# Optimization experiments

Measured on AMD Instinct MI355X. Metric: run time of the kernel, lower is better.

The kernel has to match this reference:

```python
import jax, jax.numpy as jnp
import numpy as np

N, C, H, L = 10000, 256, 8, 3
D = C // H  # per-head dim
E = 320000


def setup_inputs() -> dict:
    key = jax.random.key(0)
    ks = jax.random.split(key, 12)
    x = jax.random.normal(ks[0], (N, C), dtype=jnp.float32)
    edge_index = jax.random.randint(ks[1], (2, E), 0, N, dtype=jnp.int64)
    s = 0.02
    Wq = jax.random.normal(ks[2], (L, C, C), dtype=jnp.float32) * s
    Wk = jax.random.normal(ks[3], (L, C, C), dtype=jnp.float32) * s
    Wv = jax.random.normal(ks[4], (L, C, C), dtype=jnp.float32) * s
    Ws = jax.random.normal(ks[5], (L, C, C), dtype=jnp.float32) * s
    bq = jax.random.normal(ks[6], (L, C), dtype=jnp.float32) * s
    bk = jax.random.normal(ks[7], (L, C), dtype=jnp.float32) * s
    bv = jax.random.normal(ks[8], (L, C), dtype=jnp.float32) * s
    bs = jax.random.normal(ks[9], (L, C), dtype=jnp.float32) * s
    return {"x": x, "Wq": Wq, "bq": bq, "Wk": Wk, "bk": bk,
            "Wv": Wv, "bv": bv, "Ws": Ws, "bs": bs, "edge_index": edge_index}


def _transformer_conv(x, Wq, bq, Wk, bk, Wv, bv, Ws, bs, src, dst):
    # projections: [N, C] -> [N, H, D]
    q = (x @ Wq + bq).reshape(N, H, D)
    k = (x @ Wk + bk).reshape(N, H, D)
    v = (x @ Wv + bv).reshape(N, H, D)
    # per-edge attention scores: query at target, key/value at source
    score = jnp.einsum('ehd,ehd->eh', q[dst], k[src]) / jnp.sqrt(jnp.float32(D))  # [E, H]
    # scatter softmax over incoming edges per target node
    m = jax.ops.segment_max(score, dst, num_segments=N)            # [N, H]
    a = jnp.exp(score - m[dst])                                    # [E, H]
    denom = jax.ops.segment_sum(a, dst, num_segments=N)           # [N, H]
    alpha = a / (denom[dst] + 1e-16)                               # [E, H]
    # weighted aggregation of values
    msg = alpha[:, :, None] * v[src]                               # [E, H, D]
    out = jax.ops.segment_sum(msg, dst, num_segments=N).reshape(N, C)
    # root/skip connection
    return out + x @ Ws + bs


def reference(x, Wq, bq, Wk, bk, Wv, bv, Ws, bs, edge_index):
    src, dst = edge_index[0], edge_index[1]
    for l in range(L):
        x = _transformer_conv(x, Wq[l], bq[l], Wk[l], bk[l],
                              Wv[l], bv[l], Ws[l], bs[l], src, dst)
    return x
```

## Files before the change

### kernel.cpp

```cpp
#include <hip/hip_runtime.h>
#include <hip/hip_bf16.h>

#define N_NODES 10000
#define C_DIM   256
#define H_HEADS 8
#define D_HEAD  32
#define E_EDGES 320000
#define L_LAYERS 3
#define GN      1024

typedef __attribute__((ext_vector_type(8))) short bf16x8;
typedef __attribute__((ext_vector_type(4))) float f32x4;

__device__ __forceinline__ unsigned short f2b(float f) {
  __hip_bfloat16 h = __float2bfloat16(f);
  return *(unsigned short*)&h;
}

__device__ __forceinline__ float kv_lo(unsigned int w) {
  union { unsigned int u; float f; } c; c.u = w << 16; return c.f;
}
__device__ __forceinline__ float kv_hi(unsigned int w) {
  union { unsigned int u; float f; } c; c.u = w & 0xffff0000u; return c.f;
}

__device__ __forceinline__ float red8(float p) {
  p += __shfl_xor(p, 1);
  p += __shfl_xor(p, 2);
  p += __shfl_xor(p, 4);
  return p;
}

__device__ __forceinline__ float dot4(float4 q, uint4 w) {
  return fmaf(q.x, kv_lo(w.x),
         fmaf(q.y, kv_lo(w.y),
         fmaf(q.z, kv_lo(w.z), q.w * kv_lo(w.w))));
}

__device__ __forceinline__ void gload16(const void* g, void* l) {
  __builtin_amdgcn_global_load_lds(
      (const __attribute__((address_space(1))) unsigned int*)g,
      (__attribute__((address_space(3))) unsigned int*)l, 16, 0, 0);
}

__device__ __forceinline__ int colmap(int mat, int c) {
  if (mat == 0) return c;
  if (mat == 3) return 768 + c;
  return 256 + ((c >> 6) << 7) + ((mat - 1) << 6) + (c & 63);
}

__global__ void hist_kernel(const int* __restrict__ dst, int* __restrict__ deg) {
  int e = blockIdx.x * blockDim.x + threadIdx.x;
  if (e < E_EDGES) atomicAdd(&deg[dst[e]], 1);
}

__global__ __launch_bounds__(1024) void scan_kernel(const int* __restrict__ deg,
                                                    int* __restrict__ row_ptr) {
  __shared__ int part[1024];
  int t = threadIdx.x;
  const int CHUNK = (N_NODES + 1023) / 1024;
  int base = t * CHUNK;
  int s = 0;
  for (int i = 0; i < CHUNK; ++i) {
    int idx = base + i;
    if (idx < N_NODES) s += deg[idx];
  }
  part[t] = s;
  __syncthreads();
  for (int off = 1; off < 1024; off <<= 1) {
    int v = (t >= off) ? part[t - off] : 0;
    __syncthreads();
    part[t] += v;
    __syncthreads();
  }
  int run = (t == 0) ? 0 : part[t - 1];
  for (int i = 0; i < CHUNK; ++i) {
    int idx = base + i;
    if (idx <= N_NODES) {
      row_ptr[idx] = run;
      if (idx < N_NODES) run += deg[idx];
    }
  }
}

__global__ void scatter_kernel(const int* __restrict__ src, const int* __restrict__ dst,
                               const int* __restrict__ row_ptr, int* __restrict__ fill,
                               int* __restrict__ srcs) {
  int e = blockIdx.x * blockDim.x + threadIdx.x;
  if (e < E_EDGES) {
    int d = dst[e];
    int pos = atomicAdd(&fill[d], 1);
    srcs[row_ptr[d] + pos] = src[e];
  }
}

__global__ __launch_bounds__(256) void conv_all_kernel(
    const float* __restrict__ x, __hip_bfloat16* __restrict__ xb,
    const float* __restrict__ Wq, const float* __restrict__ Wk,
    const float* __restrict__ Wv, const float* __restrict__ Ws,
    __hip_bfloat16* __restrict__ Wt,
    const float* __restrict__ bq, const float* __restrict__ bk,
    const float* __restrict__ bv, const float* __restrict__ bs,
    float* __restrict__ biasf) {
  __shared__ float tt[32][33];
  int b = blockIdx.x, t = threadIdx.x;
  if (b < 2500) {
    int i = b * 256 + t;
    float4 f = *(const float4*)&x[(size_t)i * 4];
    union { unsigned short u[4]; uint2 w; } o;
    o.u[0] = f2b(f.x); o.u[1] = f2b(f.y); o.u[2] = f2b(f.z); o.u[3] = f2b(f.w);
    *(uint2*)&xb[(size_t)i * 4] = o.w;
  } else if (b < 3268) {
    int zz = b - 2500;
    int z = zz >> 6, tile = zz & 63;
    int l = z >> 2, mat = z & 3;
    const float* W = (mat == 0 ? Wq : mat == 1 ? Wk : mat == 2 ? Wv : Ws)
                     + (size_t)l * C_DIM * C_DIM;
    int k0 = (tile >> 3) * 32, c0 = (tile & 7) * 32;
    int tx = t & 31, ty = t >> 5;
    for (int i = 0; i < 32; i += 8)
      tt[ty + i][tx] = W[(k0 + ty + i) * C_DIM + c0 + tx];
    __syncthreads();
    for (int i = 0; i < 32; i += 8) {
      int ncol = colmap(mat, c0 + ty + i);
      Wt[(size_t)l * GN * C_DIM + (size_t)ncol * C_DIM + k0 + tx] =
          __float2bfloat16(tt[tx][ty + i]);
    }
  } else {
    int i = (b - 3268) * 256 + t;
    if (i < L_LAYERS * GN) {
      int l = i >> 10, n = i & 1023;
      int mat = n >> 8, c = n & 255;
      const float* bb = (mat == 0 ? bq : mat == 1 ? bk : mat == 2 ? bv : bs);
      biasf[l * GN + colmap(mat, c)] = bb[l * C_DIM + c];
    }
  }
}

__global__ __launch_bounds__(256) void gemm_kernel(
    const __hip_bfloat16* __restrict__ xb,
    const __hip_bfloat16* __restrict__ Wt,
    const float* __restrict__ biasf,
    float* __restrict__ q4,
    unsigned short* __restrict__ kvu,
    float* __restrict__ skip) {
  __shared__ __align__(16) unsigned short SH[16384];
  __hip_bfloat16* As = (__hip_bfloat16*)SH;
  __hip_bfloat16* Bs = (__hip_bfloat16*)(SH + 8192);
  int tid = threadIdx.x;
  int wid = tid >> 6, lane = tid & 63;
  int row0 = blockIdx.x * 128;
  int col0 = blockIdx.y * 128;
  int wr = wid >> 1, wc = wid & 1;
  int lr = lane & 15, lq = lane >> 4;
  int swz = (lr & 7) * 8;

  f32x4 acc[4][4] = {};

  for (int k0 = 0; k0 < C_DIM; k0 += 64) {
#pragma unroll
    for (int j = 0; j < 4; ++j) {
      int c = j * 256 + wid * 64 + lane;
      int arow = c >> 3;
      int kc = 8 * ((c & 7) ^ ((c >> 3) & 7));
      int grow = row0 + arow;
      if (grow > N_NODES - 1) grow = N_NODES - 1;
      gload16(xb + (size_t)grow * C_DIM + k0 + kc, As + (size_t)(j * 256 + wid * 64) * 8);
    }
#pragma unroll
    for (int j = 0; j < 4; ++j) {
      int c = j * 256 + wid * 64 + lane;
      int brow = c >> 3;
      int kc = 8 * ((c & 7) ^ ((c >> 3) & 7));
      gload16(Wt + (size_t)(col0 + brow) * C_DIM + k0 + kc,
              Bs + (size_t)(j * 256 + wid * 64) * 8);
    }
    __syncthreads();

#pragma unroll
    for (int ks = 0; ks < 2; ++ks) {
      bf16x8 fa[4], fb[4];
#pragma unroll
      for (int m = 0; m < 4; ++m)
        fa[m] = *(const bf16x8*)&As[(wr * 64 + m * 16 + lr) * 64 + ((ks * 32 + lq * 8) ^ swz)];
#pragma unroll
      for (int n = 0; n < 4; ++n)
        fb[n] = *(const bf16x8*)&Bs[(wc * 64 + n * 16 + lr) * 64 + ((ks * 32 + lq * 8) ^ swz)];
#pragma unroll
      for (int m = 0; m < 4; ++m)
#pragma unroll
        for (int n = 0; n < 4; ++n)
          acc[m][n] = __builtin_amdgcn_mfma_f32_16x16x32_bf16(fa[m], fb[n], acc[m][n], 0, 0, 0);
    }
    __syncthreads();
  }

  float bias_n[4];
#pragma unroll
  for (int n = 0; n < 4; ++n) bias_n[n] = biasf[col0 + wc * 64 + n * 16 + lr];

  if (col0 >= 256 && col0 < 768) {
    int half = wc;
#pragma unroll
    for (int m = 0; m < 4; ++m) {
#pragma unroll
      for (int n = 0; n < 4; ++n) {
        int chs = n * 16 + lr;
#pragma unroll
        for (int r = 0; r < 4; ++r) {
          int row = wr * 64 + m * 16 + lq * 4 + r;
          SH[row * 128 + chs * 2 + half] = f2b(acc[m][n][r] + bias_n[n]);
        }
      }
    }
    __syncthreads();
    int slice = (col0 - 256) >> 7;
    unsigned int* kvd = (unsigned int*)kvu;
    int t16 = tid & 15, rbase = tid >> 4;
#pragma unroll
    for (int it = 0; it < 8; ++it) {
      int row = it * 16 + rbase;
      int grow = row0 + row;
      if (grow < N_NODES) {
        uint4 vv = *(const uint4*)&SH[row * 128 + t16 * 8];
        *(uint4*)&kvd[((size_t)slice * N_NODES + grow) * 64 + t16 * 4] = vv;
      }
    }
  } else {
#pragma unroll
    for (int m = 0; m < 4; ++m) {
#pragma unroll
      for (int n = 0; n < 4; ++n) {
        int colG = col0 + wc * 64 + n * 16 + lr;
#pragma unroll
        for (int r = 0; r < 4; ++r) {
          int grow = row0 + wr * 64 + m * 16 + lq * 4 + r;
          if (grow < N_NODES) {
            float val = acc[m][n][r] + bias_n[n];
            if (col0 < 256) {
              q4[((size_t)(colG >> 6) * N_NODES + grow) * 64 + (colG & 63)] = val;
            } else {
              skip[(size_t)grow * C_DIM + (colG - 768)] = val;
            }
          }
        }
      }
    }
  }
}

__global__ __launch_bounds__(256) void agg_kernel(
    const float* __restrict__ q4,
    const unsigned int* __restrict__ kv4,
    const int* __restrict__ row_ptr, const int* __restrict__ srcs,
    float* __restrict__ out, __hip_bfloat16* __restrict__ xb_next) {
  int b = blockIdx.x;
  int u = b >> 3, r = b & 7;
  int slice = r >> 1;
  int wid = threadIdx.x >> 6, lane = threadIdx.x & 63;
  int n = ((((u << 1) | (r & 1)) << 2) + wid);
  int slot = lane >> 4;
  int l4 = (lane & 15) * 4;
  const size_t SB = (size_t)slice * N_NODES * 64;
  const float scl = 0.25503526f;

  float4 qv = *(const float4*)&q4[SB + (size_t)n * 64 + l4];
  qv.x *= scl; qv.y *= scl; qv.z *= scl; qv.w *= scl;
  const unsigned int* kvs = kv4 + SB;

  int beg = row_ptr[n], end = row_ptr[n + 1];
  float l = 0.f;
  float4 a = make_float4(0.f, 0.f, 0.f, 0.f);

  int i = beg;
  int sa, sb;
  if (i + 8 <= end) { sa = srcs[i + slot]; sb = srcs[i + 4 + slot]; }
  while (i + 8 <= end) {
    uint4 wa = *(const uint4*)&kvs[(size_t)sa * 64 + l4];
    uint4 wb = *(const uint4*)&kvs[(size_t)sb * 64 + l4];
    i += 8;
    if (i + 8 <= end) {
      sa = srcs[i + slot]; sb = srcs[i + 4 + slot];
    }
    float pa = red8(dot4(qv, wa));
    float pb = red8(dot4(qv, wb));
    float ea = exp2f(pa), eb = exp2f(pb);
    l += ea + eb;
    a.x = fmaf(ea, kv_hi(wa.x), fmaf(eb, kv_hi(wb.x), a.x));
    a.y = fmaf(ea, kv_hi(wa.y), fmaf(eb, kv_hi(wb.y), a.y));
    a.z = fmaf(ea, kv_hi(wa.z), fmaf(eb, kv_hi(wb.z), a.z));
    a.w = fmaf(ea, kv_hi(wa.w), fmaf(eb, kv_hi(wb.w), a.w));
  }
  for (; i < end; i += 4) {
    int j = i + slot;
    bool valid = j < end;
    int s = srcs[valid ? j : beg];
    uint4 w = *(const uint4*)&kvs[(size_t)s * 64 + l4];
    float p = red8(dot4(qv, w));
    float e = valid ? exp2f(p) : 0.f;
    l += e;
    a.x = fmaf(e, kv_hi(w.x), a.x);
    a.y = fmaf(e, kv_hi(w.y), a.y);
    a.z = fmaf(e, kv_hi(w.z), a.z);
    a.w = fmaf(e, kv_hi(w.w), a.w);
  }

#pragma unroll
  for (int mask = 16; mask <= 32; mask <<= 1) {
    l   += __shfl_xor(l, mask);
    a.x += __shfl_xor(a.x, mask);
    a.y += __shfl_xor(a.y, mask);
    a.z += __shfl_xor(a.z, mask);
    a.w += __shfl_xor(a.w, mask);
  }

  if (lane < 16) {
    float inv = 1.f / (l + 1e-16f);
    size_t idx = (size_t)n * C_DIM + slice * 64 + l4;
    float4 o = *(const float4*)&out[idx];
    o.x += a.x * inv; o.y += a.y * inv; o.z += a.z * inv; o.w += a.w * inv;
    *(float4*)&out[idx] = o;
    union { unsigned short us[4]; uint2 w; } ob;
    ob.us[0] = f2b(o.x); ob.us[1] = f2b(o.y); ob.us[2] = f2b(o.z); ob.us[3] = f2b(o.w);
    *(uint2*)&xb_next[idx] = ob.w;
  }
}

extern "C" void kernel_launch(void* const* d_in, const int* in_sizes, int n_in,
                              void* d_out, int out_size, void* d_ws, size_t ws_size,
                              hipStream_t stream) {
  const float* x0 = (const float*)d_in[0];
  const float* Wq = (const float*)d_in[1];
  const float* bq = (const float*)d_in[2];
  const float* Wk = (const float*)d_in[3];
  const float* bk = (const float*)d_in[4];
  const float* Wv = (const float*)d_in[5];
  const float* bv = (const float*)d_in[6];
  const float* Ws = (const float*)d_in[7];
  const float* bs = (const float*)d_in[8];
  const int* ei  = (const int*)d_in[9];
  const int* src = ei;
  const int* dst = ei + E_EDGES;
  float* out = (float*)d_out;

  const size_t NC = (size_t)N_NODES * C_DIM;
  __hip_bfloat16* xb = (__hip_bfloat16*)d_ws;
  unsigned int* kvbuf = (unsigned int*)(xb + NC);
  __hip_bfloat16* Wt = (__hip_bfloat16*)(kvbuf + NC);
  float* qbuf  = (float*)(Wt + (size_t)L_LAYERS * GN * C_DIM);
  float* skipA = qbuf + NC;
  float* biasf = skipA + NC;
  int* row_ptr = (int*)(biasf + L_LAYERS * GN);
  int* deg  = row_ptr + (N_NODES + 1);
  int* fill = deg + N_NODES;
  int* srcs = fill + N_NODES;

  hipMemsetAsync(deg, 0, 2 * N_NODES * sizeof(int), stream);
  hist_kernel<<<(E_EDGES + 255) / 256, 256, 0, stream>>>(dst, deg);
  scan_kernel<<<1, 1024, 0, stream>>>(deg, row_ptr);
  scatter_kernel<<<(E_EDGES + 255) / 256, 256, 0, stream>>>(src, dst, row_ptr, fill, srcs);

  conv_all_kernel<<<3281, 256, 0, stream>>>(x0, xb, Wq, Wk, Wv, Ws, Wt,
                                            bq, bk, bv, bs, biasf);

  for (int l = 0; l < L_LAYERS; ++l) {
    float* skip = (l == L_LAYERS - 1) ? out : skipA;
    gemm_kernel<<<dim3((N_NODES + 127) / 128, GN / 128), 256, 0, stream>>>(
        xb, Wt + (size_t)l * GN * C_DIM, biasf + l * GN, qbuf,
        (unsigned short*)kvbuf, skip);
    agg_kernel<<<dim3(N_NODES), 256, 0, stream>>>(
        qbuf, kvbuf, row_ptr, srcs, skip, xb);
  }
}
```

Baseline: 209.2 us.

## Split K/V and Q into per-head slices, shrink edge indices to 16-bit

Reorganizes the Q and packed K/V buffers from four 64-channel slices to eight 32-channel per-head slices. The aggregation kernel now gives each wave one node and one head, handling 8 edges per pass with 8 lanes each, and launches twice as many blocks. Source indices in the CSR are stored as 16-bit values, and the streaming loads and stores of q, srcs and out use nontemporal hints. The aim is more parallelism and less index and gather traffic, at the cost of smaller gather rows per edge and more blocks that each re-read the node's edge list.

New measurement: 271.1 us. 1.3x slower.

```diff
diff --git a/kernel.cpp b/kernel.cpp
--- a/kernel.cpp
+++ b/kernel.cpp
@@ -85,12 +85,12 @@
 
 __global__ void scatter_kernel(const int* __restrict__ src, const int* __restrict__ dst,
                                const int* __restrict__ row_ptr, int* __restrict__ fill,
-                               int* __restrict__ srcs) {
+                               unsigned short* __restrict__ srcs) {
   int e = blockIdx.x * blockDim.x + threadIdx.x;
   if (e < E_EDGES) {
     int d = dst[e];
     int pos = atomicAdd(&fill[d], 1);
-    srcs[row_ptr[d] + pos] = src[e];
+    srcs[row_ptr[d] + pos] = (unsigned short)src[e];
   }
 }
 
@@ -141,7 +141,7 @@
     const __hip_bfloat16* __restrict__ xb,
     const __hip_bfloat16* __restrict__ Wt,
     const float* __restrict__ biasf,
-    float* __restrict__ q4,
+    float* __restrict__ q8,
     unsigned short* __restrict__ kvu,
     float* __restrict__ skip) {
   __shared__ __align__(16) unsigned short SH[16384];
@@ -214,7 +214,7 @@
       }
     }
     __syncthreads();
-    int slice = (col0 - 256) >> 7;
+    int s2 = ((col0 - 256) >> 7) * 2;
     unsigned int* kvd = (unsigned int*)kvu;
     int t16 = tid & 15, rbase = tid >> 4;
 #pragma unroll
@@ -223,7 +223,8 @@
       int grow = row0 + row;
       if (grow < N_NODES) {
         uint4 vv = *(const uint4*)&SH[row * 128 + t16 * 8];
-        *(uint4*)&kvd[((size_t)slice * N_NODES + grow) * 64 + t16 * 4] = vv;
+        int sl8 = s2 + (t16 >> 3);
+        *(uint4*)&kvd[((size_t)sl8 * N_NODES + grow) * 32 + (t16 & 7) * 4] = vv;
       }
     }
   } else {
@@ -238,7 +239,7 @@
           if (grow < N_NODES) {
             float val = acc[m][n][r] + bias_n[n];
             if (col0 < 256) {
-              q4[((size_t)(colG >> 6) * N_NODES + grow) * 64 + (colG & 63)] = val;
+              q8[((size_t)(colG >> 5) * N_NODES + grow) * 32 + (colG & 31)] = val;
             } else {
               skip[(size_t)grow * C_DIM + (colG - 768)] = val;
             }
@@ -250,23 +251,22 @@
 }
 
 __global__ __launch_bounds__(256) void agg_kernel(
-    const float* __restrict__ q4,
-    const unsigned int* __restrict__ kv4,
-    const int* __restrict__ row_ptr, const int* __restrict__ srcs,
+    const float* __restrict__ q8,
+    const unsigned int* __restrict__ kv8,
+    const int* __restrict__ row_ptr, const unsigned short* __restrict__ srcs,
     float* __restrict__ out, __hip_bfloat16* __restrict__ xb_next) {
   int b = blockIdx.x;
-  int u = b >> 3, r = b & 7;
-  int slice = r >> 1;
+  int slice = b & 7;
   int wid = threadIdx.x >> 6, lane = threadIdx.x & 63;
-  int n = ((((u << 1) | (r & 1)) << 2) + wid);
-  int slot = lane >> 4;
-  int l4 = (lane & 15) * 4;
-  const size_t SB = (size_t)slice * N_NODES * 64;
+  int n = (b >> 3) * 4 + wid;
+  int slot = lane >> 3;
+  int l4 = (lane & 7) * 4;
+  const unsigned int* kvs = kv8 + (size_t)slice * N_NODES * 32;
   const float scl = 0.25503526f;
 
-  float4 qv = *(const float4*)&q4[SB + (size_t)n * 64 + l4];
-  qv.x *= scl; qv.y *= scl; qv.z *= scl; qv.w *= scl;
-  const unsigned int* kvs = kv4 + SB;
+  f32x4 qt = __builtin_nontemporal_load(
+      (const f32x4*)&q8[((size_t)slice * N_NODES + n) * 32 + l4]);
+  float4 qv = make_float4(qt.x * scl, qt.y * scl, qt.z * scl, qt.w * scl);
 
   int beg = row_ptr[n], end = row_ptr[n + 1];
   float l = 0.f;
@@ -274,13 +274,17 @@
 
   int i = beg;
   int sa, sb;
-  if (i + 8 <= end) { sa = srcs[i + slot]; sb = srcs[i + 4 + slot]; }
-  while (i + 8 <= end) {
-    uint4 wa = *(const uint4*)&kvs[(size_t)sa * 64 + l4];
-    uint4 wb = *(const uint4*)&kvs[(size_t)sb * 64 + l4];
-    i += 8;
-    if (i + 8 <= end) {
-      sa = srcs[i + slot]; sb = srcs[i + 4 + slot];
+  if (i + 16 <= end) {
+    sa = __builtin_nontemporal_load(srcs + i + slot);
+    sb = __builtin_nontemporal_load(srcs + i + 8 + slot);
+  }
+  while (i + 16 <= end) {
+    uint4 wa = *(const uint4*)&kvs[(size_t)sa * 32 + l4];
+    uint4 wb = *(const uint4*)&kvs[(size_t)sb * 32 + l4];
+    i += 16;
+    if (i + 16 <= end) {
+      sa = __builtin_nontemporal_load(srcs + i + slot);
+      sb = __builtin_nontemporal_load(srcs + i + 8 + slot);
     }
     float pa = red8(dot4(qv, wa));
     float pb = red8(dot4(qv, wb));
@@ -291,11 +295,11 @@
     a.z = fmaf(ea, kv_hi(wa.z), fmaf(eb, kv_hi(wb.z), a.z));
     a.w = fmaf(ea, kv_hi(wa.w), fmaf(eb, kv_hi(wb.w), a.w));
   }
-  for (; i < end; i += 4) {
+  for (; i < end; i += 8) {
     int j = i + slot;
     bool valid = j < end;
-    int s = srcs[valid ? j : beg];
-    uint4 w = *(const uint4*)&kvs[(size_t)s * 64 + l4];
+    int s = __builtin_nontemporal_load(srcs + (valid ? j : beg));
+    uint4 w = *(const uint4*)&kvs[(size_t)s * 32 + l4];
     float p = red8(dot4(qv, w));
     float e = valid ? exp2f(p) : 0.f;
     l += e;
@@ -306,7 +310,7 @@
   }
 
 #pragma unroll
-  for (int mask = 16; mask <= 32; mask <<= 1) {
+  for (int mask = 8; mask <= 32; mask <<= 1) {
     l   += __shfl_xor(l, mask);
     a.x += __shfl_xor(a.x, mask);
     a.y += __shfl_xor(a.y, mask);
@@ -314,12 +318,12 @@
     a.w += __shfl_xor(a.w, mask);
   }
 
-  if (lane < 16) {
+  if (lane < 8) {
     float inv = 1.f / (l + 1e-16f);
-    size_t idx = (size_t)n * C_DIM + slice * 64 + l4;
-    float4 o = *(const float4*)&out[idx];
+    size_t idx = (size_t)n * C_DIM + slice * 32 + l4;
+    f32x4 o = __builtin_nontemporal_load((const f32x4*)&out[idx]);
     o.x += a.x * inv; o.y += a.y * inv; o.z += a.z * inv; o.w += a.w * inv;
-    *(float4*)&out[idx] = o;
+    __builtin_nontemporal_store(o, (f32x4*)&out[idx]);
     union { unsigned short us[4]; uint2 w; } ob;
     ob.us[0] = f2b(o.x); ob.us[1] = f2b(o.y); ob.us[2] = f2b(o.z); ob.us[3] = f2b(o.w);
     *(uint2*)&xb_next[idx] = ob.w;
@@ -353,7 +357,7 @@
   int* row_ptr = (int*)(biasf + L_LAYERS * GN);
   int* deg  = row_ptr + (N_NODES + 1);
   int* fill = deg + N_NODES;
-  int* srcs = fill + N_NODES;
+  unsigned short* srcs = (unsigned short*)(fill + N_NODES);
 
   hipMemsetAsync(deg, 0, 2 * N_NODES * sizeof(int), stream);
   hist_kernel<<<(E_EDGES + 255) / 256, 256, 0, stream>>>(dst, deg);
@@ -368,7 +372,7 @@
     gemm_kernel<<<dim3((N_NODES + 127) / 128, GN / 128), 256, 0, stream>>>(
         xb, Wt + (size_t)l * GN * C_DIM, biasf + l * GN, qbuf,
         (unsigned short*)kvbuf, skip);
-    agg_kernel<<<dim3(N_NODES), 256, 0, stream>>>(
+    agg_kernel<<<dim3(20000), 256, 0, stream>>>(
         qbuf, kvbuf, row_ptr, srcs, skip, xb);
   }
 }
```

## Use one wavefront per node over full row with DPP head reductions

Applied to the files above, without the earlier changes.

Q and the packed K/V buffers now use a row-major per-node layout, so a single 64-lane wavefront reads a node's full 256-channel row in one contiguous 1KB load per edge. Before, four wavefronts each handled a 64-channel slice, each with four edge slots. The aggregation kernel walks edges serially per wavefront with uniform (readfirstlane) source indices and prefetches the next pair of rows. The 8-lane head reduction now uses DPP row operations instead of shuffles. This trades per-wave edge parallelism for better gather coalescing and fewer index loads, but gives a longer serial dependency chain per node.

New measurement: 243.1 us. 1.16x slower.

```diff
diff --git a/kernel.cpp b/kernel.cpp
--- a/kernel.cpp
+++ b/kernel.cpp
@@ -24,10 +24,16 @@
   union { unsigned int u; float f; } c; c.u = w & 0xffff0000u; return c.f;
 }
 
+template <int CTRL>
+__device__ __forceinline__ float dpp_add(float v) {
+  union { int i; float f; } c;
+  c.i = __builtin_amdgcn_update_dpp(0, __builtin_bit_cast(int, v), CTRL, 0xf, 0xf, true);
+  return v + c.f;
+}
 __device__ __forceinline__ float red8(float p) {
-  p += __shfl_xor(p, 1);
-  p += __shfl_xor(p, 2);
-  p += __shfl_xor(p, 4);
+  p = dpp_add<0xB1>(p);
+  p = dpp_add<0x4E>(p);
+  p = dpp_add<0x141>(p);
   return p;
 }
 
@@ -141,7 +147,7 @@
     const __hip_bfloat16* __restrict__ xb,
     const __hip_bfloat16* __restrict__ Wt,
     const float* __restrict__ biasf,
-    float* __restrict__ q4,
+    float* __restrict__ qf,
     unsigned short* __restrict__ kvu,
     float* __restrict__ skip) {
   __shared__ __align__(16) unsigned short SH[16384];
@@ -223,7 +229,7 @@
       int grow = row0 + row;
       if (grow < N_NODES) {
         uint4 vv = *(const uint4*)&SH[row * 128 + t16 * 8];
-        *(uint4*)&kvd[((size_t)slice * N_NODES + grow) * 64 + t16 * 4] = vv;
+        *(uint4*)&kvd[(size_t)grow * C_DIM + slice * 64 + t16 * 4] = vv;
       }
     }
   } else {
@@ -238,7 +244,7 @@
           if (grow < N_NODES) {
             float val = acc[m][n][r] + bias_n[n];
             if (col0 < 256) {
-              q4[((size_t)(colG >> 6) * N_NODES + grow) * 64 + (colG & 63)] = val;
+              qf[(size_t)grow * C_DIM + colG] = val;
             } else {
               skip[(size_t)grow * C_DIM + (colG - 768)] = val;
             }
@@ -250,80 +256,67 @@
 }
 
 __global__ __launch_bounds__(256) void agg_kernel(
-    const float* __restrict__ q4,
-    const unsigned int* __restrict__ kv4,
+    const float* __restrict__ qf,
+    const unsigned int* __restrict__ kvf,
     const int* __restrict__ row_ptr, const int* __restrict__ srcs,
     float* __restrict__ out, __hip_bfloat16* __restrict__ xb_next) {
-  int b = blockIdx.x;
-  int u = b >> 3, r = b & 7;
-  int slice = r >> 1;
   int wid = threadIdx.x >> 6, lane = threadIdx.x & 63;
-  int n = ((((u << 1) | (r & 1)) << 2) + wid);
-  int slot = lane >> 4;
-  int l4 = (lane & 15) * 4;
-  const size_t SB = (size_t)slice * N_NODES * 64;
+  int n = blockIdx.x * 4 + wid;
+  int c4 = lane * 4;
   const float scl = 0.25503526f;
 
-  float4 qv = *(const float4*)&q4[SB + (size_t)n * 64 + l4];
+  float4 qv = *(const float4*)&qf[(size_t)n * C_DIM + c4];
   qv.x *= scl; qv.y *= scl; qv.z *= scl; qv.w *= scl;
-  const unsigned int* kvs = kv4 + SB;
 
   int beg = row_ptr[n], end = row_ptr[n + 1];
   float l = 0.f;
   float4 a = make_float4(0.f, 0.f, 0.f, 0.f);
 
-  int i = beg;
-  int sa, sb;
-  if (i + 8 <= end) { sa = srcs[i + slot]; sb = srcs[i + 4 + slot]; }
-  while (i + 8 <= end) {
-    uint4 wa = *(const uint4*)&kvs[(size_t)sa * 64 + l4];
-    uint4 wb = *(const uint4*)&kvs[(size_t)sb * 64 + l4];
-    i += 8;
-    if (i + 8 <= end) {
-      sa = srcs[i + slot]; sb = srcs[i + 4 + slot];
-    }
-    float pa = red8(dot4(qv, wa));
-    float pb = red8(dot4(qv, wb));
-    float ea = exp2f(pa), eb = exp2f(pb);
-    l += ea + eb;
-    a.x = fmaf(ea, kv_hi(wa.x), fmaf(eb, kv_hi(wb.x), a.x));
-    a.y = fmaf(ea, kv_hi(wa.y), fmaf(eb, kv_hi(wb.y), a.y));
-    a.z = fmaf(ea, kv_hi(wa.z), fmaf(eb, kv_hi(wb.z), a.z));
-    a.w = fmaf(ea, kv_hi(wa.w), fmaf(eb, kv_hi(wb.w), a.w));
-  }
-  for (; i < end; i += 4) {
-    int j = i + slot;
-    bool valid = j < end;
-    int s = srcs[valid ? j : beg];
-    uint4 w = *(const uint4*)&kvs[(size_t)s * 64 + l4];
-    float p = red8(dot4(qv, w));
-    float e = valid ? exp2f(p) : 0.f;
-    l += e;
-    a.x = fmaf(e, kv_hi(w.x), a.x);
-    a.y = fmaf(e, kv_hi(w.y), a.y);
-    a.z = fmaf(e, kv_hi(w.z), a.z);
-    a.w = fmaf(e, kv_hi(w.w), a.w);
-  }
-
-#pragma unroll
-  for (int mask = 16; mask <= 32; mask <<= 1) {
-    l   += __shfl_xor(l, mask);
-    a.x += __shfl_xor(a.x, mask);
-    a.y += __shfl_xor(a.y, mask);
-    a.z += __shfl_xor(a.z, mask);
-    a.w += __shfl_xor(a.w, mask);
-  }
-
-  if (lane < 16) {
-    float inv = 1.f / (l + 1e-16f);
-    size_t idx = (size_t)n * C_DIM + slice * 64 + l4;
-    float4 o = *(const float4*)&out[idx];
-    o.x += a.x * inv; o.y += a.y * inv; o.z += a.z * inv; o.w += a.w * inv;
-    *(float4*)&out[idx] = o;
-    union { unsigned short us[4]; uint2 w; } ob;
-    ob.us[0] = f2b(o.x); ob.us[1] = f2b(o.y); ob.us[2] = f2b(o.z); ob.us[3] = f2b(o.w);
-    *(uint2*)&xb_next[idx] = ob.w;
-  }
+  if (beg < end) {
+    int s0 = __builtin_amdgcn_readfirstlane(srcs[beg]);
+    int j1 = (beg + 1 < end) ? beg + 1 : beg;
+    int s1 = __builtin_amdgcn_readfirstlane(srcs[j1]);
+    uint4 w0 = *(const uint4*)&kvf[(size_t)s0 * C_DIM + c4];
+    uint4 w1 = *(const uint4*)&kvf[(size_t)s1 * C_DIM + c4];
+    int s2 = 0, s3 = 0;
+    if (beg + 2 < end) {
+      int j3 = (beg + 3 < end) ? beg + 3 : beg;
+      s2 = __builtin_amdgcn_readfirstlane(srcs[beg + 2]);
+      s3 = __builtin_amdgcn_readfirstlane(srcs[j3]);
+    }
+    for (int i = beg; i < end; i += 2) {
+      uint4 n0, n1;
+      bool more = (i + 2) < end;
+      if (more) {
+        n0 = *(const uint4*)&kvf[(size_t)s2 * C_DIM + c4];
+        n1 = *(const uint4*)&kvf[(size_t)s3 * C_DIM + c4];
+        if (i + 4 < end) {
+          int j5 = (i + 5 < end) ? i + 5 : beg;
+          s2 = __builtin_amdgcn_readfirstlane(srcs[i + 4]);
+          s3 = __builtin_amdgcn_readfirstlane(srcs[j5]);
+        }
+      }
+      float p0 = red8(dot4(qv, w0));
+      float p1 = red8(dot4(qv, w1));
+      float e0 = exp2f(p0);
+      float e1 = (i + 1 < end) ? exp2f(p1) : 0.f;
+      l += e0 + e1;
+      a.x = fmaf(e0, kv_hi(w0.x), fmaf(e1, kv_hi(w1.x), a.x));
+      a.y = fmaf(e0, kv_hi(w0.y), fmaf(e1, kv_hi(w1.y), a.y));
+      a.z = fmaf(e0, kv_hi(w0.z), fmaf(e1, kv_hi(w1.z), a.z));
+      a.w = fmaf(e0, kv_hi(w0.w), fmaf(e1, kv_hi(w1.w), a.w));
+      if (more) { w0 = n0; w1 = n1; }
+    }
+  }
+
+  float inv = 1.f / (l + 1e-16f);
+  size_t idx = (size_t)n * C_DIM + c4;
+  float4 o = *(const float4*)&out[idx];
+  o.x += a.x * inv; o.y += a.y * inv; o.z += a.z * inv; o.w += a.w * inv;
+  *(float4*)&out[idx] = o;
+  union { unsigned short us[4]; uint2 w; } ob;
+  ob.us[0] = f2b(o.x); ob.us[1] = f2b(o.y); ob.us[2] = f2b(o.z); ob.us[3] = f2b(o.w);
+  *(uint2*)&xb_next[idx] = ob.w;
 }
 
 extern "C" void kernel_launch(void* const* d_in, const int* in_sizes, int n_in,
@@ -355,7 +348,7 @@
   int* fill = deg + N_NODES;
   int* srcs = fill + N_NODES;
 
-  hipMemsetAsync(deg, 0, 2 * N_NODES * sizeof(int), stream);
+  (void)hipMemsetAsync(deg, 0, 2 * N_NODES * sizeof(int), stream);
   hist_kernel<<<(E_EDGES + 255) / 256, 256, 0, stream>>>(dst, deg);
   scan_kernel<<<1, 1024, 0, stream>>>(deg, row_ptr);
   scatter_kernel<<<(E_EDGES + 255) / 256, 256, 0, stream>>>(src, dst, row_ptr, fill, srcs);
@@ -368,7 +361,7 @@
     gemm_kernel<<<dim3((N_NODES + 127) / 128, GN / 128), 256, 0, stream>>>(
         xb, Wt + (size_t)l * GN * C_DIM, biasf + l * GN, qbuf,
         (unsigned short*)kvbuf, skip);
-    agg_kernel<<<dim3(N_NODES), 256, 0, stream>>>(
+    agg_kernel<<<dim3((N_NODES + 3) / 4), 256, 0, stream>>>(
         qbuf, kvbuf, row_ptr, srcs, skip, xb);
   }
 }
```
